# Kernel tuning notes

Measured on AMD Instinct MI355X. Metric: run time of the kernel, lower is better.

The kernel has to match this reference:

```python
import jax, jax.numpy as jnp
import numpy as np

WEIGHTS = (0.5, 1.0, 2.0)   # per-channel weights (init kwarg)
INVERTED = True             # init kwarg


def setup_inputs() -> dict:
    key = jax.random.key(0)
    B, C, H, W = 16, 3, 256, 256
    # binary flood mask: nonzero = foreground (scipy EDT measures distance to nearest zero)
    flood = jax.random.randint(key, (B, C, H, W), 0, 2).astype(jnp.float32)
    return {"flood_batch": flood}


def _edt_squared(mask):
    """Exact squared Euclidean distance transform per [H,W] slice.

    mask: bool [B,C,H,W], True = foreground (nonzero). Returns float32 [B,C,H,W]
    squared distance from each True pixel to the nearest False pixel (0 at False).
    Uses the exact separable decomposition:
      D2[r,w] = min_{r'} ( g[r',w]^2 + (r-r')^2 ),  g = 1D horizontal distance to zero.
    """
    B, C, H, W = mask.shape
    BIG = jnp.float32(H + W)  # exceeds any achievable 1D distance

    # --- pass 1: 1D distance to nearest zero along W (forward + backward scans) ---
    m = jnp.moveaxis(mask, -1, 0)  # [W,B,C,H]

    def step(carry, mm):
        d = jnp.where(mm, jnp.minimum(carry + 1.0, BIG), 0.0)
        return d, d

    init = jnp.full((B, C, H), BIG, jnp.float32)
    _, fwd = jax.lax.scan(step, init, m)
    _, bwd = jax.lax.scan(step, init, m[::-1])
    g = jnp.minimum(fwd, bwd[::-1])          # [W,B,C,H]
    g2 = jnp.moveaxis(g, 0, -1) ** 2          # [B,C,H,W]

    # --- pass 2: exact min-plus over rows (vectorized over B,C,W; scan over output row) ---
    rows = jnp.arange(H, dtype=jnp.float32)

    def row_step(_, r):
        cand = g2 + ((r - rows) ** 2)[None, None, :, None]  # [B,C,H,W]
        return None, cand.min(axis=2)                        # [B,C,W]

    _, d2 = jax.lax.scan(row_step, None, rows)  # [H,B,C,W]
    return jnp.moveaxis(d2, 0, 2)               # [B,C,H,W]


def reference(flood_batch):
    w = jnp.asarray(WEIGHTS, jnp.float32)
    dt = jnp.sqrt(_edt_squared(flood_batch != 0))            # [B,C,H,W]
    dt = dt * w[None, :, None, None]                         # per-channel weight
    mx = dt.max(axis=(2, 3), keepdims=True)                  # per-slice max
    safe = jnp.where(mx > 0, mx, 1.0)
    scaled = (mx - dt) / safe if INVERTED else dt / safe
    return jnp.where(mx > 0, scaled, dt)
```

## Files before the change

kernel.cpp:

```cpp
#include <hip/hip_runtime.h>


#define PADV 1e30f

__global__ __launch_bounds__(256) void k1_bitmask(const float* __restrict__ in,
                                                  unsigned long long* __restrict__ bits) {
    int row = blockIdx.x * 4 + (threadIdx.x >> 6);
    int lane = threadIdx.x & 63;
    const float4 m = ((const float4*)in)[(long)row * 64 + lane];

    unsigned long long b0 = __ballot(m.x == 0.f);
    unsigned long long b1 = __ballot(m.y == 0.f);
    unsigned long long b2 = __ballot(m.z == 0.f);
    unsigned long long b3 = __ballot(m.w == 0.f);
    if (lane == 0) {
        ulonglong4* dst = (ulonglong4*)(bits + (long)row * 4);
        ulonglong4 v; v.x = b0; v.y = b1; v.z = b2; v.w = b3;
        *dst = v;
    }
}

__global__ __launch_bounds__(256) void k2_colpass(const unsigned long long* __restrict__ bits,
                                                  float* __restrict__ d2out,
                                                  float* __restrict__ stripmax) {
    __shared__ unsigned long long bm[1024];
    __shared__ float tile[16 * 273];
    __shared__ float wm[4];
    int bx = blockIdx.x;
    int slice = bx >> 4;
    int w0 = (bx & 15) * 16;
    int tid = threadIdx.x;

    {
        const unsigned long long* src = bits + (long)slice * 1024;
        #pragma unroll
        for (int i = 0; i < 4; ++i) bm[i * 256 + tid] = src[i * 256 + tid];
    }
    {
        int c = tid >> 4, i = tid & 15;
        tile[c * 273 + (i < 8 ? i : 256 + i)] = PADV;
    }
    __syncthreads();

    int c = tid & 15;
    int p = w0 + c;
    int rg = tid >> 4;

    auto nz2 = [&](int row) -> float {
        int dist = 512;
        #pragma unroll
        for (int cc = 0; cc < 4; ++cc) {
            unsigned long long M = bm[row * 4 + cc];
            int q = p - cc;
            int qa = (q < 0) ? 0 : q;
            int tp = qa >> 2;
            unsigned long long Ml = (q >= 0) ? (M & (~0ull >> (63 - tp))) : 0ull;
            int tn = (q < 0) ? 0 : ((q + 3) >> 2);
            unsigned long long Mh = (tn < 64) ? (M & (~0ull << tn)) : 0ull;
            if (Ml) dist = min(dist, q - 4 * (63 - __builtin_clzll(Ml)));
            if (Mh) dist = min(dist, 4 * __builtin_ctzll(Mh) - q);
        }
        float fd = (float)dist;
        return fd * fd;
    };

    #pragma unroll
    for (int k = 0; k < 16; ++k) {
        int r = rg + 16 * k;
        tile[c * 273 + 8 + r] = nz2(r);
    }
    __syncthreads();

    int r0 = rg * 16;
    float s[32];
    #pragma unroll
    for (int i = 0; i < 32; ++i) s[i] = tile[c * 273 + r0 + i];

    float dmin[16];
    #pragma unroll
    for (int k = 0; k < 16; ++k) dmin[k] = s[k + 8];
    #pragma unroll
    for (int o = -8; o <= 8; ++o) {
        if (o == 0) continue;
        float oo = (float)(o * o);
        #pragma unroll
        for (int k = 0; k < 16; ++k)
            dmin[k] = fminf(dmin[k], s[k + 8 + o] + oo);
    }

    #pragma unroll
    for (int k = 0; k < 16; ++k) {
        if (dmin[k] > 80.0f) {
            float best = dmin[k];
            int r = r0 + k;
            for (int rp = 0; rp < 256; ++rp) {
                float dr = (float)(r - rp);
                best = fminf(best, fmaf(dr, dr, tile[c * 273 + 8 + rp]));
            }
            dmin[k] = best;
        }
    }

    float* dst = d2out + (long)slice * 65536 + w0 + c;
    float m = 0.f;
    #pragma unroll
    for (int k = 0; k < 16; ++k) {
        dst[(long)(r0 + k) * 256] = dmin[k];
        m = fmaxf(m, dmin[k]);
    }
    #pragma unroll
    for (int off = 32; off >= 1; off >>= 1)
        m = fmaxf(m, __shfl_down(m, off, 64));
    if ((tid & 63) == 0) wm[tid >> 6] = m;
    __syncthreads();
    if (tid == 0)
        stripmax[bx] = fmaxf(fmaxf(wm[0], wm[1]), fmaxf(wm[2], wm[3]));
}

__global__ __launch_bounds__(256) void k3_final(float* __restrict__ out,
                                                const float* __restrict__ stripmax) {
    __shared__ float sMx;
    int tid = threadIdx.x;
    int idx4 = blockIdx.x * 256 + tid;
    int slice = blockIdx.x >> 6;
    if (tid < 16) {
        float v = stripmax[slice * 16 + tid];
        #pragma unroll
        for (int off = 8; off >= 1; off >>= 1) v = fmaxf(v, __shfl_down(v, off, 64));
        if (tid == 0) sMx = v;
    }
    __syncthreads();

    int c = slice % 3;
    float wgt = (c == 0) ? 0.5f : ((c == 1) ? 1.0f : 2.0f);
    float mx = wgt * __builtin_sqrtf(sMx);

    float4 d2 = ((float4*)out)[idx4];
    float4 r;
    if (mx > 0.f) {
        float inv = 1.0f / mx;
        r.x = (mx - wgt * __builtin_sqrtf(d2.x)) * inv;
        r.y = (mx - wgt * __builtin_sqrtf(d2.y)) * inv;
        r.z = (mx - wgt * __builtin_sqrtf(d2.z)) * inv;
        r.w = (mx - wgt * __builtin_sqrtf(d2.w)) * inv;
    } else {
        r.x = wgt * __builtin_sqrtf(d2.x);
        r.y = wgt * __builtin_sqrtf(d2.y);
        r.z = wgt * __builtin_sqrtf(d2.z);
        r.w = wgt * __builtin_sqrtf(d2.w);
    }
    ((float4*)out)[idx4] = r;
}

extern "C" void kernel_launch(void* const* d_in, const int* in_sizes, int n_in,
                              void* d_out, int out_size, void* d_ws, size_t ws_size,
                              hipStream_t stream) {
    const float* in = (const float*)d_in[0];
    float* out = (float*)d_out;
    float* stripmax = (float*)d_ws;
    unsigned long long* bits = (unsigned long long*)((char*)d_ws + 4096);

    k1_bitmask<<<3072, 256, 0, stream>>>(in, bits);
    k2_colpass<<<768, 256, 0, stream>>>(bits, out, stripmax);
    k3_final<<<3072, 256, 0, stream>>>(out, stripmax);
}
```

Before: 83.29 us.

## Fuse bitmask construction into column pass kernel, dropping separate launch

```diff
diff --git a/kernel.cpp b/kernel.cpp
--- a/kernel.cpp
+++ b/kernel.cpp
@@ -3,38 +3,38 @@
 
 #define PADV 1e30f
 
-__global__ __launch_bounds__(256) void k1_bitmask(const float* __restrict__ in,
-                                                  unsigned long long* __restrict__ bits) {
-    int row = blockIdx.x * 4 + (threadIdx.x >> 6);
-    int lane = threadIdx.x & 63;
-    const float4 m = ((const float4*)in)[(long)row * 64 + lane];
-
-    unsigned long long b0 = __ballot(m.x == 0.f);
-    unsigned long long b1 = __ballot(m.y == 0.f);
-    unsigned long long b2 = __ballot(m.z == 0.f);
-    unsigned long long b3 = __ballot(m.w == 0.f);
-    if (lane == 0) {
-        ulonglong4* dst = (ulonglong4*)(bits + (long)row * 4);
-        ulonglong4 v; v.x = b0; v.y = b1; v.z = b2; v.w = b3;
-        *dst = v;
-    }
-}
-
-__global__ __launch_bounds__(256) void k2_colpass(const unsigned long long* __restrict__ bits,
-                                                  float* __restrict__ d2out,
-                                                  float* __restrict__ stripmax) {
+__global__ __launch_bounds__(256) void k12_colpass(const float* __restrict__ in,
+                                                   float* __restrict__ d2out,
+                                                   float* __restrict__ stripmax) {
     __shared__ unsigned long long bm[1024];
     __shared__ float tile[16 * 273];
     __shared__ float wm[4];
     int bx = blockIdx.x;
-    int slice = bx >> 4;
-    int w0 = (bx & 15) * 16;
+    int xr = bx & 7;
+    int cc_ = bx >> 3;
+    int strip = cc_ & 15;
+    int slice = (cc_ >> 4) * 8 + xr;
+    int w0 = strip * 16;
     int tid = threadIdx.x;
+    int wave = tid >> 6;
+    int lane = tid & 63;
 
     {
-        const unsigned long long* src = bits + (long)slice * 1024;
-        #pragma unroll
-        for (int i = 0; i < 4; ++i) bm[i * 256 + tid] = src[i * 256 + tid];
+        const float4* in4 = (const float4*)(in + (long)slice * 65536);
+        #pragma unroll 8
+        for (int i = 0; i < 64; ++i) {
+            int r = wave * 64 + i;
+            float4 v = in4[r * 64 + lane];
+            unsigned long long b0 = __ballot(v.x == 0.f);
+            unsigned long long b1 = __ballot(v.y == 0.f);
+            unsigned long long b2 = __ballot(v.z == 0.f);
+            unsigned long long b3 = __ballot(v.w == 0.f);
+            if (lane == 0) {
+                ulonglong4* dst = (ulonglong4*)(bm + r * 4);
+                ulonglong4 u; u.x = b0; u.y = b1; u.z = b2; u.w = b3;
+                *dst = u;
+            }
+        }
     }
     {
         int c = tid >> 4, i = tid & 15;
@@ -114,7 +114,7 @@
     if ((tid & 63) == 0) wm[tid >> 6] = m;
     __syncthreads();
     if (tid == 0)
-        stripmax[bx] = fmaxf(fmaxf(wm[0], wm[1]), fmaxf(wm[2], wm[3]));
+        stripmax[slice * 16 + strip] = fmaxf(fmaxf(wm[0], wm[1]), fmaxf(wm[2], wm[3]));
 }
 
 __global__ __launch_bounds__(256) void k3_final(float* __restrict__ out,
@@ -158,9 +158,7 @@
     const float* in = (const float*)d_in[0];
     float* out = (float*)d_out;
     float* stripmax = (float*)d_ws;
-    unsigned long long* bits = (unsigned long long*)((char*)d_ws + 4096);
 
-    k1_bitmask<<<3072, 256, 0, stream>>>(in, bits);
-    k2_colpass<<<768, 256, 0, stream>>>(bits, out, stripmax);
+    k12_colpass<<<768, 256, 0, stream>>>(in, out, stripmax);
     k3_final<<<3072, 256, 0, stream>>>(out, stripmax);
 }
```

Result: slower. 98.60 us (+18.4%).
